# Performance work log

Measured on AMD Instinct MI355X. Metric: run time of the kernel, lower is better.

## Reference

```python
import jax, jax.numpy as jnp
import numpy as np

NEG_INF = -9e15  # matches torch's -9000000000000000.0 mask value
ALPHA = 0.2      # LeakyReLU negative slope


def setup_inputs() -> dict:
    key = jax.random.key(0)
    k1, k2, k3, k4 = jax.random.split(key, 4)
    B, N, Fin, Fout = 8, 2048, 256, 256
    h = jax.random.normal(k1, (B, N, Fin), dtype=jnp.float32)
    adj = jax.random.randint(k2, (B, N, N), 0, 2, dtype=jnp.int32)
    # xavier_uniform with gain=1.414
    limW = 1.414 * np.sqrt(6.0 / (Fin + Fout))
    W = jax.random.uniform(k3, (Fin, Fout), minval=-limW, maxval=limW, dtype=jnp.float32)
    lima = 1.414 * np.sqrt(6.0 / (2 * Fout + 1))
    a = jax.random.uniform(k4, (2 * Fout, 1), minval=-lima, maxval=lima, dtype=jnp.float32)
    return {"h": h, "adj": adj, "W": W, "a": a}


def reference(h, adj, W, a):
    # h: (B, N, Fin), adj: (B, N, N), W: (Fin, Fout), a: (2*Fout, 1)
    Fout = W.shape[1]
    Wh = jnp.einsum('bni,io->bno', h, W)                 # (B, N, Fout)
    # e[b,i,j] = leakyrelu(Wh[b,i] @ a1 + Wh[b,j] @ a2) -- equivalent to the
    # original concat([Wh_i, Wh_j]) @ a without the O(N^2 * 2F) intermediate.
    e1 = Wh @ a[:Fout, 0]                                # (B, N)
    e2 = Wh @ a[Fout:, 0]                                # (B, N)
    e = jax.nn.leaky_relu(e1[:, :, None] + e2[:, None, :], negative_slope=ALPHA)
    masked = jnp.where(adj > 0, e, NEG_INF)
    attention = jax.nn.softmax(masked, axis=-1)          # (B, N, N)
    # dropout omitted (deterministic eval-mode reference)
    h_prime = jnp.einsum('bij,bjo->bio', attention, Wh)  # (B, N, Fout)
    return jax.nn.elu(h_prime), attention
```

## Files before the change

kernel.cpp:

```cpp
#include <hip/hip_runtime.h>
#include <hip/hip_bf16.h>
#include <stdint.h>

#define NEG_INF -9.0e15f
#define LRELU_ALPHA 0.2f
#define LOG2E 1.442695040888963f

using bf16x8  = __attribute__((ext_vector_type(8))) short;
using f32x4   = __attribute__((ext_vector_type(4))) float;
using short4v = __attribute__((ext_vector_type(4))) short;
using int4v   = __attribute__((ext_vector_type(4))) int;
using float4v = __attribute__((ext_vector_type(4))) float;
using uint4v  = __attribute__((ext_vector_type(4))) unsigned;

static __device__ __forceinline__ float b2f(short s) {
  unsigned u = ((unsigned)(unsigned short)s) << 16;
  return __builtin_bit_cast(float, u);
}
static __device__ __forceinline__ short f2bf(float f) {
  unsigned u = __builtin_bit_cast(unsigned, f);
  u = u + 0x7FFFu + ((u >> 16) & 1u);
  return (short)(u >> 16);
}
static __device__ __forceinline__ unsigned cvtpk_bf16(float lo, float hi) {
  unsigned r;
  asm volatile("v_cvt_pk_bf16_f32 %0, %1, %2" : "=v"(r) : "v"(lo), "v"(hi));
  return r;
}
static __device__ __forceinline__ void gload16(const void* g, void* l) {
  __builtin_amdgcn_global_load_lds((const __attribute__((address_space(1))) void*)g,
                                   (__attribute__((address_space(3))) void*)l, 16, 0, 0);
}

__global__ __launch_bounds__(256) void castT_W_kernel(
    const float* __restrict__ src, short* __restrict__ dst)
{
  __shared__ float t[64][65];
  const int m0 = blockIdx.x * 64, n0 = blockIdx.y * 64;
  const int tid = threadIdx.x;
  const int rr = tid >> 3, cc = (tid & 7) * 8;
#pragma unroll
  for (int p = 0; p < 2; ++p) {
    int row = rr + p * 32;
    const float* sp = src + (m0 + row) * 256 + n0 + cc;
    float4v v0 = *(const float4v*)sp;
    float4v v1 = *(const float4v*)(sp + 4);
#pragma unroll
    for (int j = 0; j < 4; ++j) { t[row][cc + j] = v0[j]; t[row][cc + 4 + j] = v1[j]; }
  }
  __syncthreads();
#pragma unroll
  for (int p = 0; p < 2; ++p) {
    int orow = rr + p * 32;
    short vv[8] __attribute__((aligned(16)));
#pragma unroll
    for (int j = 0; j < 8; ++j) vv[j] = f2bf(t[cc + j][orow]);
    short* dp = dst + (n0 + orow) * 256 + m0 + cc;
    *(int4v*)dp = *(const int4v*)vv;
  }
}

__global__ __launch_bounds__(256) void transpose_bf16_kernel(
    const short* __restrict__ src, short* __restrict__ dst,
    int M, int N, long long ss, long long ds)
{
  __shared__ short t[64][68];
  const int b = blockIdx.z;
  src += (long long)b * ss; dst += (long long)b * ds;
  const int m0 = blockIdx.x * 64, n0 = blockIdx.y * 64;
  const int tid = threadIdx.x;
  const int rr = tid >> 3, cc = (tid & 7) * 8;
#pragma unroll
  for (int p = 0; p < 2; ++p) {
    int row = rr + p * 32;
    const short* sp = src + (long long)(m0 + row) * N + n0 + cc;
    short4v v0 = *(const short4v*)sp;
    short4v v1 = *(const short4v*)(sp + 4);
    *(short4v*)&t[row][cc]     = v0;
    *(short4v*)&t[row][cc + 4] = v1;
  }
  __syncthreads();
#pragma unroll
  for (int p = 0; p < 2; ++p) {
    int orow = rr + p * 32;
    short vv[8] __attribute__((aligned(16)));
#pragma unroll
    for (int j = 0; j < 8; ++j) vv[j] = t[cc + j][orow];
    short* dp = dst + (long long)(n0 + orow) * M + m0 + cc;
    *(int4v*)dp = *(const int4v*)vv;
  }
}

__global__ __launch_bounds__(256) void evec_kernel(
    const short* __restrict__ Wh, const float* __restrict__ a,
    float* __restrict__ e1, float* __restrict__ e2)
{
  const int wid = threadIdx.x >> 6, lane = threadIdx.x & 63;
  const long long r = (long long)blockIdx.x * 4 + wid;
  short4v hv   = *(const short4v*)(Wh + r * 256 + lane * 4);
  float4v a1v  = *(const float4v*)(a + lane * 4);
  float4v a2v  = *(const float4v*)(a + 256 + lane * 4);
  float s1 = 0.f, s2 = 0.f;
#pragma unroll
  for (int k = 0; k < 4; ++k) {
    float x = b2f(hv[k]);
    s1 += x * a1v[k];
    s2 += x * a2v[k];
  }
#pragma unroll
  for (int off = 32; off > 0; off >>= 1) {
    s1 += __shfl_xor(s1, off, 64);
    s2 += __shfl_xor(s2, off, 64);
  }
  if (lane == 0) { e1[r] = s1; e2[r] = s2; }
}

__global__ __launch_bounds__(256) void pack_stats_kernel(
    const int* __restrict__ adj, const float* __restrict__ e1,
    const float* __restrict__ e2, unsigned char* __restrict__ mask,
    float* __restrict__ Lr, float* __restrict__ Dr)
{
  const int i = blockIdx.x;
  const int b = blockIdx.y;
  const long long row = (long long)b * 2048 + i;
  const int tid = threadIdx.x;
  const int wid = tid >> 6, lane = tid & 63;
  const int j0 = tid * 8;

  const int*   arow = adj + row * 2048 + j0;
  const float  ei   = e1[row];
  const float* e2b  = e2 + b * 2048 + j0;

  int4v   a0 = *(const int4v*)(arow);
  int4v   a1 = *(const int4v*)(arow + 4);
  float4v f0 = *(const float4v*)(e2b);
  float4v f1 = *(const float4v*)(e2b + 4);

  float s[8]; unsigned byte = 0u;
#pragma unroll
  for (int k = 0; k < 8; ++k) {
    float x = ei + (k < 4 ? f0[k] : f1[k - 4]);
    float v = fmaxf(x, LRELU_ALPHA * x);
    int  ad = (k < 4 ? a0[k] : a1[k - 4]);
    if (ad > 0) { s[k] = v; byte |= (1u << k); } else s[k] = NEG_INF;
  }
  float m = s[0];
#pragma unroll
  for (int k = 1; k < 8; ++k) m = fmaxf(m, s[k]);
#pragma unroll
  for (int off = 32; off > 0; off >>= 1) m = fmaxf(m, __shfl_xor(m, off, 64));

  __shared__ float wmax[4], wsum[4];
  if (lane == 0) wmax[wid] = m;
  __syncthreads();
  const float M = fmaxf(fmaxf(wmax[0], wmax[1]), fmaxf(wmax[2], wmax[3]));
  const bool empty = (M == NEG_INF);

  mask[row * 256 + tid] = empty ? (unsigned char)0xFF : (unsigned char)byte;

  float t = 0.f;
#pragma unroll
  for (int k = 0; k < 8; ++k) t += __expf(s[k] - M);
#pragma unroll
  for (int off = 32; off > 0; off >>= 1) t += __shfl_xor(t, off, 64);
  if (lane == 0) wsum[wid] = t;
  __syncthreads();
  if (tid == 0) {
    const float S = wsum[0] + wsum[1] + wsum[2] + wsum[3];
    Lr[row] = empty ? 0.0f : LOG2E;
    Dr[row] = empty ? -11.0f : (-M * LOG2E - __log2f(S));
  }
}

__global__ __launch_bounds__(256, 2) void fused_pv_kernel(
    const unsigned char* __restrict__ mask, const float* __restrict__ e1,
    const float* __restrict__ e2, const float* __restrict__ Lr,
    const float* __restrict__ Dr, const short* __restrict__ Bt,
    float* __restrict__ attnw, float* __restrict__ C)
{
  __shared__ short As[32 * 64];
  __shared__ short Bs[256 * 64];
  const int bid = blockIdx.x;
  const int bz  = bid & 7;
  const int M0  = (bid >> 3) << 5;
  const int tid = threadIdx.x;
  const int w = tid >> 6, lane = tid & 63;
  const int g = lane >> 4, lr = lane & 15;

  const long long rb = (long long)bz * 2048;
  Bt    += (long long)bz * 524288;
  attnw += (long long)bz * 4194304;
  C     += (long long)bz * 524288;

  const int pr = tid >> 3, kc8 = tid & 7;
  const int prow = M0 + pr;
  const float E1p = e1[rb + prow];
  const float Lp  = Lr[rb + prow];
  const float Dp  = Dr[rb + prow];
  const unsigned char* mrow = mask + (rb + prow) * 256;
  float* arow = attnw + (long long)prow * 2048;
  short* as_wr = As + pr * 64 + ((kc8 ^ (pr & 7)) << 3);
  const float* e2b = e2 + rb;

  const int bcol_off = lane >> 3;
  const int bchunk   = (lane & 7) ^ ((lane >> 3) & 7);

  f32x4 acc[2][4] = {};

  for (int k0 = 0; k0 < 2048; k0 += 64) {
    __syncthreads();
    {
      const unsigned by = mrow[(k0 >> 3) + kc8];
      const int kk = k0 + kc8 * 8;
      float4v eo = *(const float4v*)(e2b + kk);
      float4v eh = *(const float4v*)(e2b + kk + 4);
      float p[8];
#pragma unroll
      for (int e = 0; e < 8; ++e) {
        float x = E1p + (e < 4 ? eo[e] : eh[e - 4]);
        float v = fmaxf(x, LRELU_ALPHA * x);
        float P = __builtin_amdgcn_exp2f(fmaf(v, Lp, Dp));
        p[e] = ((by >> e) & 1u) ? P : 0.0f;
      }
      float4v o0, o1;
#pragma unroll
      for (int e = 0; e < 4; ++e) { o0[e] = p[e]; o1[e] = p[e + 4]; }
      *(float4v*)(arow + kk)     = o0;
      *(float4v*)(arow + kk + 4) = o1;
      uint4v uv;
      uv[0] = cvtpk_bf16(p[0], p[1]);
      uv[1] = cvtpk_bf16(p[2], p[3]);
      uv[2] = cvtpk_bf16(p[4], p[5]);
      uv[3] = cvtpk_bf16(p[6], p[7]);
      *(bf16x8*)as_wr = __builtin_bit_cast(bf16x8, uv);
    }
#pragma unroll
    for (int q = 0; q < 8; ++q) {
      int pp = w * 8 + q;
      int col = pp * 8 + bcol_off;
      gload16(Bt + (long long)col * 2048 + k0 + bchunk * 8, Bs + pp * 512);
    }
    __syncthreads();

    bf16x8 af[2][2], bfr[4][2];
#pragma unroll
    for (int i = 0; i < 2; ++i) {
      int row = i * 16 + lr;
#pragma unroll
      for (int s = 0; s < 2; ++s)
        af[i][s] = *(const bf16x8*)(As + row * 64 + (((s * 4 + g) ^ (row & 7)) << 3));
    }
#pragma unroll
    for (int j = 0; j < 4; ++j) {
      int col = w * 64 + j * 16 + lr;
#pragma unroll
      for (int s = 0; s < 2; ++s)
        bfr[j][s] = *(const bf16x8*)(Bs + col * 64 + (((s * 4 + g) ^ (col & 7)) << 3));
    }
#pragma unroll
    for (int s = 0; s < 2; ++s)
#pragma unroll
      for (int i = 0; i < 2; ++i)
#pragma unroll
        for (int j = 0; j < 4; ++j)
          acc[i][j] = __builtin_amdgcn_mfma_f32_16x16x32_bf16(af[i][s], bfr[j][s], acc[i][j], 0, 0, 0);
  }

#pragma unroll
  for (int i = 0; i < 2; ++i) {
    int row_base = M0 + i * 16 + 4 * g;
#pragma unroll
    for (int j = 0; j < 4; ++j) {
      int col = w * 64 + j * 16 + lr;
#pragma unroll
      for (int r = 0; r < 4; ++r) {
        float v = acc[i][j][r];
        v = (v > 0.f) ? v : (__expf(v) - 1.f);
        C[(long long)(row_base + r) * 256 + col] = v;
      }
    }
  }
}

__global__ __launch_bounds__(256) void gemm_h_kernel(
    const float* __restrict__ A, const short* __restrict__ Bt,
    short* __restrict__ C, int N, int K)
{
  __shared__ short As[128 * 32];
  __shared__ short Bs[128 * 32];
  const int m0 = blockIdx.x * 128, n0 = blockIdx.y * 128;
  const int tid = threadIdx.x;
  const int w = tid >> 6, lane = tid & 63;
  const int wr = w >> 1, wc = w & 1;
  const int g = lane >> 4, lr = lane & 15;

  f32x4 acc[4][4] = {};

  for (int k0 = 0; k0 < K; k0 += 32) {
    __syncthreads();
#pragma unroll
    for (int q = 0; q < 2; ++q) {
      int c = q * 256 + tid;
      int row = c >> 2, kq = (c & 3) << 3;
      const float* ap = A + (long long)(m0 + row) * K + k0 + kq;
      float4v u0 = *(const float4v*)ap;
      float4v u1 = *(const float4v*)(ap + 4);
      uint4v uv;
      uv[0] = cvtpk_bf16(u0[0], u0[1]);
      uv[1] = cvtpk_bf16(u0[2], u0[3]);
      uv[2] = cvtpk_bf16(u1[0], u1[1]);
      uv[3] = cvtpk_bf16(u1[2], u1[3]);
      *(bf16x8*)(As + c * 8) = __builtin_bit_cast(bf16x8, uv);
    }
#pragma unroll
    for (int q = 0; q < 2; ++q) {
      int p = w * 2 + q;
      int c = p * 64 + lane;
      int row = c >> 2, kq = (c & 3) << 3;
      gload16(Bt + (long long)(n0 + row) * K + k0 + kq, Bs + p * 512);
    }
    __syncthreads();

    bf16x8 af[4], bfr[4];
#pragma unroll
    for (int i = 0; i < 4; ++i) {
      af[i]  = *(const bf16x8*)(As + (wr * 64 + i * 16 + lr) * 32 + 8 * g);
      bfr[i] = *(const bf16x8*)(Bs + (wc * 64 + i * 16 + lr) * 32 + 8 * g);
    }
#pragma unroll
    for (int i = 0; i < 4; ++i)
#pragma unroll
      for (int j = 0; j < 4; ++j)
        acc[i][j] = __builtin_amdgcn_mfma_f32_16x16x32_bf16(af[i], bfr[j], acc[i][j], 0, 0, 0);
  }

#pragma unroll
  for (int i = 0; i < 4; ++i) {
    int row_base = m0 + wr * 64 + i * 16 + 4 * g;
#pragma unroll
    for (int j = 0; j < 4; ++j) {
      int col = n0 + wc * 64 + j * 16 + lr;
#pragma unroll
      for (int r = 0; r < 4; ++r)
        C[(long long)(row_base + r) * N + col] = f2bf(acc[i][j][r]);
    }
  }
}

extern "C" void kernel_launch(void* const* d_in, const int* in_sizes, int n_in,
                              void* d_out, int out_size, void* d_ws, size_t ws_size,
                              hipStream_t stream)
{
  const float* h   = (const float*)d_in[0];
  const int*   adj = (const int*)d_in[1];
  const float* W   = (const float*)d_in[2];
  const float* a   = (const float*)d_in[3];

  float* hp_out   = (float*)d_out;
  float* attn_out = hp_out + 4194304LL;

  unsigned char* mask = (unsigned char*)d_ws;
  short* W_t  = (short*)(mask + 4194304);
  short* Wh   = W_t + 65536;
  short* Wh_t = Wh + 4194304;
  float* e1   = (float*)(Wh_t + 4194304);
  float* e2   = e1 + 16384;
  float* Lr   = e2 + 16384;
  float* Dr   = Lr + 16384;

  castT_W_kernel<<<dim3(4, 4), 256, 0, stream>>>(W, W_t);
  gemm_h_kernel<<<dim3(128, 2, 1), 256, 0, stream>>>(h, W_t, Wh, 256, 256);
  transpose_bf16_kernel<<<dim3(32, 4, 8), 256, 0, stream>>>(Wh, Wh_t, 2048, 256, 524288LL, 524288LL);
  evec_kernel<<<4096, 256, 0, stream>>>(Wh, a, e1, e2);
  pack_stats_kernel<<<dim3(2048, 8), 256, 0, stream>>>(adj, e1, e2, mask, Lr, Dr);
  fused_pv_kernel<<<512, 256, 0, stream>>>(mask, e1, e2, Lr, Dr, Wh_t, attn_out, hp_out);
}
```

Before: 125.0 us.

## Double-buffer LDS tiles in PV kernel to overlap loads with MFMA

Adds a second pair of shared-memory buffers for the probability and Wh tiles in the attention-times-V kernel and software-pipelines the k loop. The next tile is staged (global loads, exp computation, attention writes) while MFMAs run on the current tile, and one barrier per step replaces two. This is meant to hide global-load and exp latency behind matrix math, at the cost of doubling LDS use (about 72KB per block), which may reduce occupancy below the two blocks per CU requested.

```diff
diff --git a/kernel.cpp b/kernel.cpp
--- a/kernel.cpp
+++ b/kernel.cpp
@@ -172,14 +172,14 @@
   }
 }
 
-__global__ __launch_bounds__(256, 2) void fused_pv_kernel(
+__global__ __launch_bounds__(256, 2) void pv_kernel(
     const unsigned char* __restrict__ mask, const float* __restrict__ e1,
     const float* __restrict__ e2, const float* __restrict__ Lr,
     const float* __restrict__ Dr, const short* __restrict__ Bt,
     float* __restrict__ attnw, float* __restrict__ C)
 {
-  __shared__ short As[32 * 64];
-  __shared__ short Bs[256 * 64];
+  __shared__ short As0[32 * 64],  As1[32 * 64];
+  __shared__ short Bs0[256 * 64], Bs1[256 * 64];
   const int bid = blockIdx.x;
   const int bz  = bid & 7;
   const int M0  = (bid >> 3) << 5;
@@ -199,7 +199,7 @@
   const float Dp  = Dr[rb + prow];
   const unsigned char* mrow = mask + (rb + prow) * 256;
   float* arow = attnw + (long long)prow * 2048;
-  short* as_wr = As + pr * 64 + ((kc8 ^ (pr & 7)) << 3);
+  const int as_off = pr * 64 + ((kc8 ^ (pr & 7)) << 3);
   const float* e2b = e2 + rb;
 
   const int bcol_off = lane >> 3;
@@ -207,55 +207,53 @@
 
   f32x4 acc[2][4] = {};
 
-  for (int k0 = 0; k0 < 2048; k0 += 64) {
-    __syncthreads();
-    {
-      const unsigned by = mrow[(k0 >> 3) + kc8];
-      const int kk = k0 + kc8 * 8;
-      float4v eo = *(const float4v*)(e2b + kk);
-      float4v eh = *(const float4v*)(e2b + kk + 4);
-      float p[8];
-#pragma unroll
-      for (int e = 0; e < 8; ++e) {
-        float x = E1p + (e < 4 ? eo[e] : eh[e - 4]);
-        float v = fmaxf(x, LRELU_ALPHA * x);
-        float P = __builtin_amdgcn_exp2f(fmaf(v, Lp, Dp));
-        p[e] = ((by >> e) & 1u) ? P : 0.0f;
-      }
-      float4v o0, o1;
-#pragma unroll
-      for (int e = 0; e < 4; ++e) { o0[e] = p[e]; o1[e] = p[e + 4]; }
-      *(float4v*)(arow + kk)     = o0;
-      *(float4v*)(arow + kk + 4) = o1;
-      uint4v uv;
-      uv[0] = cvtpk_bf16(p[0], p[1]);
-      uv[1] = cvtpk_bf16(p[2], p[3]);
-      uv[2] = cvtpk_bf16(p[4], p[5]);
-      uv[3] = cvtpk_bf16(p[6], p[7]);
-      *(bf16x8*)as_wr = __builtin_bit_cast(bf16x8, uv);
-    }
+  auto STAGE = [&](short* BsD, short* AsD, int k0) {
 #pragma unroll
     for (int q = 0; q < 8; ++q) {
       int pp = w * 8 + q;
       int col = pp * 8 + bcol_off;
-      gload16(Bt + (long long)col * 2048 + k0 + bchunk * 8, Bs + pp * 512);
-    }
-    __syncthreads();
-
+      gload16(Bt + (long long)col * 2048 + k0 + bchunk * 8, BsD + pp * 512);
+    }
+    const unsigned by = mrow[(k0 >> 3) + kc8];
+    const int kk = k0 + kc8 * 8;
+    float4v eo = *(const float4v*)(e2b + kk);
+    float4v eh = *(const float4v*)(e2b + kk + 4);
+    float p[8];
+#pragma unroll
+    for (int e = 0; e < 8; ++e) {
+      float x = E1p + (e < 4 ? eo[e] : eh[e - 4]);
+      float v = fmaxf(x, LRELU_ALPHA * x);
+      float P = __builtin_amdgcn_exp2f(fmaf(v, Lp, Dp));
+      p[e] = ((by >> e) & 1u) ? P : 0.0f;
+    }
+    float4v o0, o1;
+#pragma unroll
+    for (int e = 0; e < 4; ++e) { o0[e] = p[e]; o1[e] = p[e + 4]; }
+    *(float4v*)(arow + kk)     = o0;
+    *(float4v*)(arow + kk + 4) = o1;
+    uint4v uv;
+    uv[0] = cvtpk_bf16(p[0], p[1]);
+    uv[1] = cvtpk_bf16(p[2], p[3]);
+    uv[2] = cvtpk_bf16(p[4], p[5]);
+    uv[3] = cvtpk_bf16(p[6], p[7]);
+    *(bf16x8*)(AsD + as_off) = __builtin_bit_cast(bf16x8, uv);
+  };
+
+  auto COMPUTE = [&](const short* BsD, const short* AsD) {
     bf16x8 af[2][2], bfr[4][2];
 #pragma unroll
     for (int i = 0; i < 2; ++i) {
       int row = i * 16 + lr;
 #pragma unroll
       for (int s = 0; s < 2; ++s)
-        af[i][s] = *(const bf16x8*)(As + row * 64 + (((s * 4 + g) ^ (row & 7)) << 3));
+        af[i][s] = *(const bf16x8*)(AsD + row * 64 + (((s * 4 + g) ^ (row & 7)) << 3));
     }
 #pragma unroll
     for (int j = 0; j < 4; ++j) {
       int col = w * 64 + j * 16 + lr;
 #pragma unroll
       for (int s = 0; s < 2; ++s)
-        bfr[j][s] = *(const bf16x8*)(Bs + col * 64 + (((s * 4 + g) ^ (col & 7)) << 3));
+        bfr[j][s] = *(const bf16x8*)(BsD + col * 64 + (((s * 4 + g) ^ (col & 7)) << 3));
     }
 #pragma unroll
     for (int s = 0; s < 2; ++s)
@@ -264,6 +262,17 @@
 #pragma unroll
         for (int j = 0; j < 4; ++j)
           acc[i][j] = __builtin_amdgcn_mfma_f32_16x16x32_bf16(af[i][s], bfr[j][s], acc[i][j], 0, 0, 0);
+  };
+
+  STAGE(Bs0, As0, 0);
+  __syncthreads();
+  for (int t = 0; t < 32; t += 2) {
+    STAGE(Bs1, As1, (t + 1) * 64);
+    COMPUTE(Bs0, As0);
+    __syncthreads();
+    if (t + 2 < 32) STAGE(Bs0, As0, (t + 2) * 64);
+    COMPUTE(Bs1, As1);
+    __syncthreads();
   }
 
 #pragma unroll
@@ -373,5 +382,5 @@
   transpose_bf16_kernel<<<dim3(32, 4, 8), 256, 0, stream>>>(Wh, Wh_t, 2048, 256, 524288LL, 524288LL);
   evec_kernel<<<4096, 256, 0, stream>>>(Wh, a, e1, e2);
   pack_stats_kernel<<<dim3(2048, 8), 256, 0, stream>>>(adj, e1, e2, mask, Lr, Dr);
-  fused_pv_kernel<<<512, 256, 0, stream>>>(mask, e1, e2, Lr, Dr, Wh_t, attn_out, hp_out);
-}
+  pv_kernel<<<512, 256, 0, stream>>>(mask, e1, e2, Lr, Dr, Wh_t, attn_out, hp_out);
+}
```

New measurement: 120.6 us. -3.5%, faster.
